# Optimization experiments

Measured on AMD Instinct MI355X. Metric: run time of the kernel, lower is better.

## Reference

```python
import jax, jax.numpy as jnp
import numpy as np

MEM_SLOTS, NUM_HEADS, HEAD_SIZE, KEY_SIZE = 8, 8, 128, 128
MEM_SIZE = NUM_HEADS * HEAD_SIZE  # 1024
NUM_GATES = 2 * MEM_SIZE          # 2048 (gate_style='unit')
B, T, INPUT_SIZE = 128, 32, 1024


def _ln(x, g, b, eps=1e-5):
    m = x.mean(-1, keepdims=True)
    v = ((x - m) ** 2).mean(-1, keepdims=True)
    return (x - m) / jnp.sqrt(v + eps) * g + b


def setup_inputs() -> dict:
    key = jax.random.key(0)
    ks = jax.random.split(key, 12)
    s = 0.02  # weight init scale
    memory = jnp.tile(jnp.eye(MEM_SLOTS, MEM_SIZE, dtype=jnp.float32)[None], (B, 1, 1))
    return {
        'x': jax.random.normal(ks[0], (B, T, INPUT_SIZE), jnp.float32),
        'memory': memory,
        'Wi': s * jax.random.normal(ks[1], (INPUT_SIZE, MEM_SIZE), jnp.float32),
        'bi': jnp.zeros((MEM_SIZE,), jnp.float32),
        'Wq': s * jax.random.normal(ks[2], (MEM_SIZE, KEY_SIZE * NUM_HEADS), jnp.float32),
        'bq': jnp.zeros((KEY_SIZE * NUM_HEADS,), jnp.float32),
        'Wk': s * jax.random.normal(ks[3], (MEM_SIZE, KEY_SIZE * NUM_HEADS), jnp.float32),
        'bk': jnp.zeros((KEY_SIZE * NUM_HEADS,), jnp.float32),
        'Wv': s * jax.random.normal(ks[4], (MEM_SIZE, HEAD_SIZE * NUM_HEADS), jnp.float32),
        'bv': jnp.zeros((HEAD_SIZE * NUM_HEADS,), jnp.float32),
        'Wm': s * jax.random.normal(ks[5], (MEM_SIZE, MEM_SIZE), jnp.float32),
        'bm': jnp.zeros((MEM_SIZE,), jnp.float32),
        'ln1_g': jnp.ones((MEM_SIZE,), jnp.float32),
        'ln1_b': jnp.zeros((MEM_SIZE,), jnp.float32),
        'ln2_g': jnp.ones((MEM_SIZE,), jnp.float32),
        'ln2_b': jnp.zeros((MEM_SIZE,), jnp.float32),
        'rep_w': jax.random.normal(ks[6], (MEM_SIZE,), jnp.float32),
        'Wg': s * jax.random.normal(ks[7], (MEM_SIZE, NUM_GATES), jnp.float32),
        'bg': jnp.zeros((NUM_GATES,), jnp.float32),
        'Wmg': 0.01 * jax.random.normal(ks[8], (MEM_SLOTS, MEM_SIZE, NUM_GATES), jnp.float32),
        'forget_bias': jnp.asarray(1.0, jnp.float32),
        'input_bias': jnp.asarray(0.0, jnp.float32),
    }


def reference(x, memory, Wi, bi, Wq, bq, Wk, bk, Wv, bv, Wm, bm,
              ln1_g, ln1_b, ln2_g, ln2_b, rep_w, Wg, bg, Wmg,
              forget_bias, input_bias):
    Bx, S, D, H, K = x.shape[0], MEM_SLOTS, MEM_SIZE, NUM_HEADS, KEY_SIZE

    def step(mem, xt):                             # mem: (B,S,D), xt: (B,input)
        inp = xt @ Wi + bi                         # input_projector -> (B,D)
        inp_r = inp[:, None, :]                    # (B,1,D)
        # --- multihead attention: q from memory, k/v from projected input ---
        q = (mem @ Wq + bq).reshape(Bx, S, H, K).transpose(0, 2, 1, 3)   # (B,H,S,K)
        k = (inp_r @ Wk + bk).reshape(Bx, 1, H, K).transpose(0, 2, 1, 3)  # (B,H,1,K)
        v = (inp_r @ Wv + bv).reshape(Bx, 1, H, HEAD_SIZE).transpose(0, 2, 1, 3)
        scores = jax.nn.softmax(jnp.einsum('bhsk,bhtk->bhst', q, k), axis=-1)  # unscaled, per source
        att = jnp.einsum('bhst,bhtd->bhsd', scores, v)
        att = att.transpose(0, 2, 1, 3).reshape(Bx, S, D)
        # --- residual + LN, shared-weight 2-layer relu MLP, residual + LN ---
        m1 = _ln(mem + att, ln1_g, ln1_b)
        h = jax.nn.relu(m1 @ Wm + bm)
        h = jax.nn.relu(h @ Wm + bm)               # ModuleList([l]*2) shares weights
        m2 = _ln(m1 + h, ln2_g, ln2_b)
        # --- gates (computed from OLD memory and projected input) ---
        gi = (jax.nn.relu(rep_w * inp_r).mean(axis=1) @ Wg + bg)[:, None, :]  # RepeatLinear
        gm = jnp.einsum('bsd,sdg->bsg', jnp.tanh(mem), Wmg)                    # GroupLinearLayer
        gates = gm + gi                                                        # (B,S,2D)
        ig, fg = jnp.split(gates, 2, axis=-1)
        ig = jax.nn.sigmoid(ig + input_bias)
        fg = jax.nn.sigmoid(fg + forget_bias)
        new_mem = ig * jnp.tanh(m2) + fg * mem
        return new_mem, new_mem.reshape(Bx, S * D)

    final_mem, outs = jax.lax.scan(step, memory, x.transpose(1, 0, 2))
    return outs, final_mem  # outs: (T,B,S*D)
```

## Files before the change

### kernel.cpp

```cpp
#include <hip/hip_runtime.h>
#include <math.h>

#define DMEM   1024
#define NGATES 2048
#define NB     128
#define NT     32

__device__ inline float sigm(float x) { return 1.f / (1.f + __expf(-x)); }

template<int FOLD>
__device__ __forceinline__ void gemm128_core(
    const float* __restrict__ A, int lda, long psA,
    const float* __restrict__ abias,
    const float* __restrict__ rep,
    const float* __restrict__ W, int ldw,
    const float* __restrict__ bias,
    float* __restrict__ C, int ldc,
    int row0, int col0, int kbeg, int kend,
    float (*As)[132], float (*Bs)[132])
{
    const int tid  = threadIdx.x;
    const int tr   = (tid >> 4) << 2, tc = (tid & 15) << 2;
    const int arow = tid >> 1, ah = (tid & 1) * 8;
    const int brow = tid >> 4, bcol = (tid & 15) * 8;

    float4 a0, a1, b0, b1;
    auto LOAD = [&](int k0) {
        const float* ap = A + (long)(row0 + arow) * lda + k0 + ah;
        a0 = *(const float4*)ap;
        a1 = *(const float4*)(ap + 4);
        if (FOLD) {
            float4 p0 = *(const float4*)(ap + psA);
            float4 p1 = *(const float4*)(ap + psA + 4);
            float4 c0 = *(const float4*)(abias + k0 + ah);
            float4 c1 = *(const float4*)(abias + k0 + ah + 4);
            a0.x += p0.x + c0.x; a0.y += p0.y + c0.y;
            a0.z += p0.z + c0.z; a0.w += p0.w + c0.w;
            a1.x += p1.x + c1.x; a1.y += p1.y + c1.y;
            a1.z += p1.z + c1.z; a1.w += p1.w + c1.w;
        }
        if (rep) {
            float4 r0 = *(const float4*)(rep + k0 + ah);
            float4 r1 = *(const float4*)(rep + k0 + ah + 4);
            a0.x = fmaxf(a0.x * r0.x, 0.f); a0.y = fmaxf(a0.y * r0.y, 0.f);
            a0.z = fmaxf(a0.z * r0.z, 0.f); a0.w = fmaxf(a0.w * r0.w, 0.f);
            a1.x = fmaxf(a1.x * r1.x, 0.f); a1.y = fmaxf(a1.y * r1.y, 0.f);
            a1.z = fmaxf(a1.z * r1.z, 0.f); a1.w = fmaxf(a1.w * r1.w, 0.f);
        }
        const float* bp = W + (long)(k0 + brow) * ldw + col0 + bcol;
        b0 = *(const float4*)bp;
        b1 = *(const float4*)(bp + 4);
    };

    float acc[8][8] = {};
    LOAD(kbeg);
    const int NIT = (kend - kbeg) >> 4;
    for (int it = 0; it < NIT; ++it) {
        __syncthreads();
        As[ah + 0][arow] = a0.x; As[ah + 1][arow] = a0.y;
        As[ah + 2][arow] = a0.z; As[ah + 3][arow] = a0.w;
        As[ah + 4][arow] = a1.x; As[ah + 5][arow] = a1.y;
        As[ah + 6][arow] = a1.z; As[ah + 7][arow] = a1.w;
        *(float4*)&Bs[brow][bcol]     = b0;
        *(float4*)&Bs[brow][bcol + 4] = b1;
        __syncthreads();
        if (it + 1 < NIT) LOAD(kbeg + ((it + 1) << 4));
#pragma unroll
        for (int kk = 0; kk < 16; ++kk) {
            float a[8], b[8];
            *(float4*)&a[0] = *(const float4*)&As[kk][tr];
            *(float4*)&a[4] = *(const float4*)&As[kk][64 + tr];
            *(float4*)&b[0] = *(const float4*)&Bs[kk][tc];
            *(float4*)&b[4] = *(const float4*)&Bs[kk][64 + tc];
#pragma unroll
            for (int i = 0; i < 8; ++i)
#pragma unroll
                for (int j = 0; j < 8; ++j)
                    acc[i][j] = fmaf(a[i], b[j], acc[i][j]);
        }
    }

#pragma unroll
    for (int jh = 0; jh < 2; ++jh) {
        int cbase = col0 + jh * 64 + tc;
        float4 bv = make_float4(0.f, 0.f, 0.f, 0.f);
        if (bias) bv = *(const float4*)&bias[cbase];
#pragma unroll
        for (int ih = 0; ih < 2; ++ih) {
#pragma unroll
            for (int i = 0; i < 4; ++i) {
                int row = row0 + ih * 64 + tr + i;
                *(float4*)(C + (long)row * ldc + cbase) =
                    make_float4(acc[ih * 4 + i][jh * 4 + 0] + bv.x,
                                acc[ih * 4 + i][jh * 4 + 1] + bv.y,
                                acc[ih * 4 + i][jh * 4 + 2] + bv.z,
                                acc[ih * 4 + i][jh * 4 + 3] + bv.w);
            }
        }
    }
}

__global__ __launch_bounds__(256)
void gemm_inp(const float* __restrict__ x, const float* __restrict__ Wi,
              float* __restrict__ inpP)
{
    __shared__ float As[16][132];
    __shared__ float Bs[16][132];
    const int bid = blockIdx.x;
    const int kc = bid >> 8, j = bid & 255;
    gemm128_core<0>(x, 1024, 0, nullptr, nullptr, Wi, 1024, nullptr,
                    inpP + (long)kc * 4194304, 1024,
                    (j >> 3) * 128, (j & 7) * 128, kc * 512, kc * 512 + 512,
                    As, Bs);
}

__global__ __launch_bounds__(256)
void vgi_kern(const float* __restrict__ inpP, const float* __restrict__ bi,
              const float* __restrict__ repw,
              const float* __restrict__ Wv, const float* __restrict__ bv,
              float* __restrict__ v,
              const float* __restrict__ Wg, const float* __restrict__ bg,
              float* __restrict__ gi)
{
    __shared__ float As[16][132];
    __shared__ float Bs[16][132];
    const int bid = blockIdx.x;
    const bool isv = bid < 256;
    const int  j   = isv ? bid : bid - 256;
    const int  row0 = isv ? (j >> 3) * 128 : (j >> 4) * 128;
    const int  col0 = isv ? (j & 7) * 128  : (j & 15) * 128;
    gemm128_core<1>(inpP, 1024, 4194304, bi,
                    isv ? nullptr : repw,
                    isv ? Wv : Wg, isv ? 1024 : 2048,
                    isv ? bv : bg,
                    isv ? v : gi, isv ? 1024 : 2048,
                    row0, col0, 0, 1024, As, Bs);
}

template<int AMODE>
__device__ __forceinline__ void gemm64_core(
    const float* __restrict__ A, int lda, long psA,
    const float* __restrict__ abias,
    const float* __restrict__ W, int ldw,
    float* __restrict__ C, int ldc,
    int row0, int col0, int kbeg, int kend,
    float (*As)[68], float (*Bs)[68])
{
    const int tid  = threadIdx.x;
    const int tr   = (tid >> 4) << 2, tc = (tid & 15) << 2;
    const int arow = tid >> 2, aseg = (tid & 3) * 8;
    const int brow = tid >> 3, bcol = (tid & 7) * 8;

    float4 a0, a1, b0, b1;
    auto LOAD = [&](int k0) {
        const float* ap = A + (long)(row0 + arow) * lda + k0 + aseg;
        if (AMODE == 0) {
            a0 = *(const float4*)ap;
            a1 = *(const float4*)(ap + 4);
        } else {
            float4 p0 = *(const float4*)ap;
            float4 p1 = *(const float4*)(ap + psA);
            float4 q0 = *(const float4*)(ap + 4);
            float4 q1 = *(const float4*)(ap + psA + 4);
            float4 c0 = *(const float4*)(abias + k0 + aseg);
            float4 c1 = *(const float4*)(abias + k0 + aseg + 4);
            a0.x = fmaxf(p0.x + p1.x + c0.x, 0.f);
            a0.y = fmaxf(p0.y + p1.y + c0.y, 0.f);
            a0.z = fmaxf(p0.z + p1.z + c0.z, 0.f);
            a0.w = fmaxf(p0.w + p1.w + c0.w, 0.f);
            a1.x = fmaxf(q0.x + q1.x + c1.x, 0.f);
            a1.y = fmaxf(q0.y + q1.y + c1.y, 0.f);
            a1.z = fmaxf(q0.z + q1.z + c1.z, 0.f);
            a1.w = fmaxf(q0.w + q1.w + c1.w, 0.f);
        }
        const float* bp = W + (long)(k0 + brow) * ldw + col0 + bcol;
        b0 = *(const float4*)bp;
        b1 = *(const float4*)(bp + 4);
    };

    float acc[4][4] = {};
    LOAD(kbeg);
    const int NIT = (kend - kbeg) >> 5;
    for (int it = 0; it < NIT; ++it) {
        __syncthreads();
        As[aseg + 0][arow] = a0.x; As[aseg + 1][arow] = a0.y;
        As[aseg + 2][arow] = a0.z; As[aseg + 3][arow] = a0.w;
        As[aseg + 4][arow] = a1.x; As[aseg + 5][arow] = a1.y;
        As[aseg + 6][arow] = a1.z; As[aseg + 7][arow] = a1.w;
        *(float4*)&Bs[brow][bcol]     = b0;
        *(float4*)&Bs[brow][bcol + 4] = b1;
        __syncthreads();
        if (it + 1 < NIT) LOAD(kbeg + ((it + 1) << 5));
#pragma unroll
        for (int kk = 0; kk < 32; ++kk) {
            float4 av = *(const float4*)&As[kk][tr];
            float4 bv = *(const float4*)&Bs[kk][tc];
            acc[0][0] = fmaf(av.x, bv.x, acc[0][0]); acc[0][1] = fmaf(av.x, bv.y, acc[0][1]);
            acc[0][2] = fmaf(av.x, bv.z, acc[0][2]); acc[0][3] = fmaf(av.x, bv.w, acc[0][3]);
            acc[1][0] = fmaf(av.y, bv.x, acc[1][0]); acc[1][1] = fmaf(av.y, bv.y, acc[1][1]);
            acc[1][2] = fmaf(av.y, bv.z, acc[1][2]); acc[1][3] = fmaf(av.y, bv.w, acc[1][3]);
            acc[2][0] = fmaf(av.z, bv.x, acc[2][0]); acc[2][1] = fmaf(av.z, bv.y, acc[2][1]);
            acc[2][2] = fmaf(av.z, bv.z, acc[2][2]); acc[2][3] = fmaf(av.z, bv.w, acc[2][3]);
            acc[3][0] = fmaf(av.w, bv.x, acc[3][0]); acc[3][1] = fmaf(av.w, bv.y, acc[3][1]);
            acc[3][2] = fmaf(av.w, bv.z, acc[3][2]); acc[3][3] = fmaf(av.w, bv.w, acc[3][3]);
        }
    }

#pragma unroll
    for (int i = 0; i < 4; ++i)
        *(float4*)(C + (long)(row0 + tr + i) * ldc + col0 + tc) =
            make_float4(acc[i][0], acc[i][1], acc[i][2], acc[i][3]);
}

template<int LVL>
__global__ __launch_bounds__(256)
void step_gemms(const float* __restrict__ m1, const float* __restrict__ Wm,
                const float* __restrict__ bm,
                float* __restrict__ hP, float* __restrict__ h2P,
                const float* __restrict__ tm, const float* __restrict__ Wmg,
                float* __restrict__ gm)
{
    __shared__ float As[32][68];
    __shared__ float Bs[32][68];
    const int bid = blockIdx.x;
    if (bid < 512) {
        int x = bid & 15, y = (bid >> 4) & 15, kc = bid >> 8;
        if (LVL == 0)
            gemm64_core<0>(m1, 1024, 0, nullptr, Wm, 1024,
                           hP + (long)kc * 1048576, 1024,
                           y * 64, x * 64, kc * 512, kc * 512 + 512, As, Bs);
        else
            gemm64_core<1>(hP, 1024, 1048576, bm, Wm, 1024,
                           h2P + (long)kc * 1048576, 1024,
                           y * 64, x * 64, kc * 512, kc * 512 + 512, As, Bs);
    } else {
        int j = bid - 512;
        int x = (j & 15) + (LVL == 0 ? 0 : 16);
        int y = (j >> 4) & 1, s = j >> 5;
        gemm64_core<0>(tm + s * 1024, 8192, 0, nullptr,
                       Wmg + (long)s * 2097152, 2048,
                       gm + s * 2048, 16384,
                       y * 64, x * 64, 0, 1024, As, Bs);
    }
}

__device__ inline void block_reduce2(float& s1, float& s2)
{
    __shared__ float red[2][4];
    __syncthreads();
#pragma unroll
    for (int off = 32; off > 0; off >>= 1) {
        s1 += __shfl_down(s1, off, 64);
        s2 += __shfl_down(s2, off, 64);
    }
    int tid = threadIdx.x;
    if ((tid & 63) == 0) { red[0][tid >> 6] = s1; red[1][tid >> 6] = s2; }
    __syncthreads();
    s1 = red[0][0] + red[0][1] + red[0][2] + red[0][3];
    s2 = red[1][0] + red[1][1] + red[1][2] + red[1][3];
}

__global__ __launch_bounds__(256)
void ln1_kern(const float* __restrict__ memprev, const float* __restrict__ v,
              const float* __restrict__ g, const float* __restrict__ bb,
              float* __restrict__ m1, float* __restrict__ tm)
{
    const int row = blockIdx.x;
    const int b   = row >> 3;
    const int d   = threadIdx.x << 2;

    float4 mv = *(const float4*)(memprev + (long)row * DMEM + d);
    float4 vv = *(const float4*)(v + ((long)b * NT) * DMEM + d);

    *(float4*)(tm + (long)row * DMEM + d) =
        make_float4(tanhf(mv.x), tanhf(mv.y), tanhf(mv.z), tanhf(mv.w));

    float x0 = mv.x + vv.x, x1 = mv.y + vv.y, x2 = mv.z + vv.z, x3 = mv.w + vv.w;
    float s1 = x0 + x1 + x2 + x3;
    float s2 = x0 * x0 + x1 * x1 + x2 * x2 + x3 * x3;
    block_reduce2(s1, s2);
    float mean = s1 * (1.f / 1024.f);
    float var  = s2 * (1.f / 1024.f) - mean * mean;
    float inv  = 1.f / sqrtf(var + 1e-5f);

    float4 gg = *(const float4*)&g[d];
    float4 bv = *(const float4*)&bb[d];
    *(float4*)(m1 + (long)row * DMEM + d) =
        make_float4((x0 - mean) * inv * gg.x + bv.x,
                    (x1 - mean) * inv * gg.y + bv.y,
                    (x2 - mean) * inv * gg.z + bv.z,
                    (x3 - mean) * inv * gg.w + bv.w);
}

__global__ __launch_bounds__(256)
void step_fused(const float* m1in, const float* __restrict__ h2P,
                const float* __restrict__ bm,
                const float* __restrict__ g2, const float* __restrict__ b2,
                const float* __restrict__ gm, const float* __restrict__ gi, int t,
                const float* __restrict__ memprev,
                const float* __restrict__ fbp, const float* __restrict__ ibp,
                const float* __restrict__ v,
                const float* __restrict__ g1, const float* __restrict__ b1,
                float* __restrict__ outp, float* m1out,
                float* __restrict__ tm, int last)
{
    const int row = blockIdx.x;
    const int b   = row >> 3;
    const int d   = threadIdx.x << 2;
    const long o  = (long)row * DMEM + d;

    float4 a  = *(const float4*)(m1in + o);
    float4 q0 = *(const float4*)(h2P + o);
    float4 q1 = *(const float4*)(h2P + 1048576 + o);
    float4 bb = *(const float4*)&bm[d];
    float x0 = a.x + fmaxf(q0.x + q1.x + bb.x, 0.f);
    float x1 = a.y + fmaxf(q0.y + q1.y + bb.y, 0.f);
    float x2 = a.z + fmaxf(q0.z + q1.z + bb.z, 0.f);
    float x3 = a.w + fmaxf(q0.w + q1.w + bb.w, 0.f);

    float s1 = x0 + x1 + x2 + x3;
    float s2 = x0 * x0 + x1 * x1 + x2 * x2 + x3 * x3;
    block_reduce2(s1, s2);
    float mean = s1 * (1.f / 1024.f);
    float var  = s2 * (1.f / 1024.f) - mean * mean;
    float inv  = 1.f / sqrtf(var + 1e-5f);

    float4 gg = *(const float4*)&g2[d];
    float4 b2v = *(const float4*)&b2[d];
    float t20 = tanhf((x0 - mean) * inv * gg.x + b2v.x);
    float t21 = tanhf((x1 - mean) * inv * gg.y + b2v.y);
    float t22 = tanhf((x2 - mean) * inv * gg.z + b2v.z);
    float t23 = tanhf((x3 - mean) * inv * gg.w + b2v.w);

    const float ib = *ibp, fb = *fbp;
    const long go = (long)row * NGATES + d;
    float4 ge0 = *(const float4*)(gm + go);
    float4 ge1 = *(const float4*)(gm + go + DMEM);
    const long io = ((long)b * NT + t) * NGATES + d;
    float4 i0 = *(const float4*)(gi + io);
    float4 i1 = *(const float4*)(gi + io + DMEM);
    float4 mv = *(const float4*)(memprev + o);

    float4 out;
    out.x = sigm(ge0.x + i0.x + ib) * t20 + sigm(ge1.x + i1.x + fb) * mv.x;
    out.y = sigm(ge0.y + i0.y + ib) * t21 + sigm(ge1.y + i1.y + fb) * mv.y;
    out.z = sigm(ge0.z + i0.z + ib) * t22 + sigm(ge1.z + i1.z + fb) * mv.z;
    out.w = sigm(ge0.w + i0.w + ib) * t23 + sigm(ge1.w + i1.w + fb) * mv.w;
    *(float4*)(outp + o) = out;

    if (!last) {
        float4 vv = *(const float4*)(v + ((long)b * NT + t + 1) * DMEM + d);
        *(float4*)(tm + o) =
            make_float4(tanhf(out.x), tanhf(out.y), tanhf(out.z), tanhf(out.w));

        float y0 = out.x + vv.x, y1 = out.y + vv.y;
        float y2 = out.z + vv.z, y3 = out.w + vv.w;
        float u1 = y0 + y1 + y2 + y3;
        float u2 = y0 * y0 + y1 * y1 + y2 * y2 + y3 * y3;
        block_reduce2(u1, u2);
        float mean1 = u1 * (1.f / 1024.f);
        float var1  = u2 * (1.f / 1024.f) - mean1 * mean1;
        float inv1  = 1.f / sqrtf(var1 + 1e-5f);

        float4 g1v = *(const float4*)&g1[d];
        float4 b1v = *(const float4*)&b1[d];
        *(float4*)(m1out + o) =
            make_float4((y0 - mean1) * inv1 * g1v.x + b1v.x,
                        (y1 - mean1) * inv1 * g1v.y + b1v.y,
                        (y2 - mean1) * inv1 * g1v.z + b1v.z,
                        (y3 - mean1) * inv1 * g1v.w + b1v.w);
    }
}

extern "C" void kernel_launch(void* const* d_in, const int* in_sizes, int n_in,
                              void* d_out, int out_size, void* d_ws, size_t ws_size,
                              hipStream_t stream)
{
    const float* x    = (const float*)d_in[0];
    const float* mem0 = (const float*)d_in[1];
    const float* Wi   = (const float*)d_in[2];
    const float* bi   = (const float*)d_in[3];
    const float* Wv   = (const float*)d_in[8];
    const float* bv   = (const float*)d_in[9];
    const float* Wm   = (const float*)d_in[10];
    const float* bm   = (const float*)d_in[11];
    const float* ln1g = (const float*)d_in[12];
    const float* ln1b = (const float*)d_in[13];
    const float* ln2g = (const float*)d_in[14];
    const float* ln2b = (const float*)d_in[15];
    const float* repw = (const float*)d_in[16];
    const float* Wg   = (const float*)d_in[17];
    const float* bg   = (const float*)d_in[18];
    const float* Wmg  = (const float*)d_in[19];
    const float* fbp  = (const float*)d_in[20];
    const float* ibp  = (const float*)d_in[21];

    float* out = (float*)d_out;
    char*  ws  = (char*)d_ws;
    const long MB = 1024L * 1024L;

    float* v    = (float*)(ws + 0 * MB);
    float* gi   = (float*)(ws + 16 * MB);
    float* inpP = (float*)(ws + 48 * MB);
    float* m1   = (float*)(ws + 48 * MB);
    float* tm   = (float*)(ws + 52 * MB);
    float* hP   = (float*)(ws + 56 * MB);
    float* gm   = (float*)(ws + 64 * MB);
    float* h2P  = (float*)(ws + 72 * MB);

    dim3 blk(256);

    gemm_inp<<<512, blk, 0, stream>>>(x, Wi, inpP);
    vgi_kern<<<768, blk, 0, stream>>>(inpP, bi, repw, Wv, bv, v, Wg, bg, gi);

    ln1_kern<<<1024, blk, 0, stream>>>(mem0, v, ln1g, ln1b, m1, tm);

    const long stepN = (long)NB * 8 * DMEM;
    for (int t = 0; t < NT; ++t) {
        const float* memprev = (t == 0) ? mem0 : out + (long)(t - 1) * stepN;

        step_gemms<0><<<768, blk, 0, stream>>>(m1, Wm, bm, hP, h2P, tm, Wmg, gm);
        step_gemms<1><<<768, blk, 0, stream>>>(m1, Wm, bm, hP, h2P, tm, Wmg, gm);
        step_fused<<<1024, blk, 0, stream>>>(
            m1, h2P, bm, ln2g, ln2b, gm, gi, t, memprev, fbp, ibp,
            v, ln1g, ln1b, out + (long)t * stepN, m1, tm,
            (t == NT - 1) ? 1 : 0);
    }

    hipMemcpyAsync(out + 32L * stepN, out + 31L * stepN, stepN * sizeof(float),
                   hipMemcpyDeviceToDevice, stream);
}
```

Before: 5.283 ms.

## Replace per-step kernel launches with a persistent cooperative kernel using grid syncs

Runs the whole 32-step recurrence inside one cooperative kernel of 768 blocks. Grid-wide barriers separate the two GEMM phases and the LayerNorm/gate tail, replacing 96 separate kernel launches. The final-memory copy is folded into the last step's tail writes instead of a separate memcpy. The cost is grid.sync overhead, tail rows spread unevenly over blocks (1024 rows on 768 blocks), and a fallback to the old launches if the cooperative launch fails.

```diff
diff --git a/kernel.cpp b/kernel.cpp
--- a/kernel.cpp
+++ b/kernel.cpp
@@ -1,10 +1,14 @@
 #include <hip/hip_runtime.h>
+#include <hip/hip_cooperative_groups.h>
 #include <math.h>
+
+namespace cg = cooperative_groups;
 
 #define DMEM   1024
 #define NGATES 2048
 #define NB     128
 #define NT     32
+#define STEPN  1048576L
 
 __device__ inline float sigm(float x) { return 1.f / (1.f + __expf(-x)); }
 
@@ -212,6 +216,205 @@
             make_float4(acc[i][0], acc[i][1], acc[i][2], acc[i][3]);
 }
 
+__device__ inline void block_reduce2(float& s1, float& s2)
+{
+    __shared__ float red[2][4];
+    __syncthreads();
+#pragma unroll
+    for (int off = 32; off > 0; off >>= 1) {
+        s1 += __shfl_down(s1, off, 64);
+        s2 += __shfl_down(s2, off, 64);
+    }
+    int tid = threadIdx.x;
+    if ((tid & 63) == 0) { red[0][tid >> 6] = s1; red[1][tid >> 6] = s2; }
+    __syncthreads();
+    s1 = red[0][0] + red[0][1] + red[0][2] + red[0][3];
+    s2 = red[1][0] + red[1][1] + red[1][2] + red[1][3];
+}
+
+__global__ __launch_bounds__(256)
+void ln1_kern(const float* __restrict__ memprev, const float* __restrict__ v,
+              const float* __restrict__ g, const float* __restrict__ bb,
+              float* __restrict__ m1, float* __restrict__ tm)
+{
+    const int row = blockIdx.x;
+    const int b   = row >> 3;
+    const int d   = threadIdx.x << 2;
+
+    float4 mv = *(const float4*)(memprev + (long)row * DMEM + d);
+    float4 vv = *(const float4*)(v + ((long)b * NT) * DMEM + d);
+
+    *(float4*)(tm + (long)row * DMEM + d) =
+        make_float4(tanhf(mv.x), tanhf(mv.y), tanhf(mv.z), tanhf(mv.w));
+
+    float x0 = mv.x + vv.x, x1 = mv.y + vv.y, x2 = mv.z + vv.z, x3 = mv.w + vv.w;
+    float s1 = x0 + x1 + x2 + x3;
+    float s2 = x0 * x0 + x1 * x1 + x2 * x2 + x3 * x3;
+    block_reduce2(s1, s2);
+    float mean = s1 * (1.f / 1024.f);
+    float var  = s2 * (1.f / 1024.f) - mean * mean;
+    float inv  = 1.f / sqrtf(var + 1e-5f);
+
+    float4 gg = *(const float4*)&g[d];
+    float4 bv = *(const float4*)&bb[d];
+    *(float4*)(m1 + (long)row * DMEM + d) =
+        make_float4((x0 - mean) * inv * gg.x + bv.x,
+                    (x1 - mean) * inv * gg.y + bv.y,
+                    (x2 - mean) * inv * gg.z + bv.z,
+                    (x3 - mean) * inv * gg.w + bv.w);
+}
+
+__device__ __forceinline__ void tail_row(
+    int row, int t, const float* __restrict__ m1in,
+    const float* __restrict__ h2P, const float* __restrict__ bm,
+    const float* __restrict__ g2, const float* __restrict__ b2,
+    const float* __restrict__ gm, const float* __restrict__ gi,
+    const float* __restrict__ memprev, float fb, float ib,
+    const float* __restrict__ v,
+    const float* __restrict__ g1, const float* __restrict__ b1,
+    float* __restrict__ outp, float* m1out, float* __restrict__ tm,
+    int last, float* __restrict__ outFinal)
+{
+    const int b = row >> 3;
+    const int d = threadIdx.x << 2;
+    const long o = (long)row * DMEM + d;
+
+    float4 a  = *(const float4*)(m1in + o);
+    float4 q0 = *(const float4*)(h2P + o);
+    float4 q1 = *(const float4*)(h2P + 1048576 + o);
+    float4 bb = *(const float4*)&bm[d];
+    float x0 = a.x + fmaxf(q0.x + q1.x + bb.x, 0.f);
+    float x1 = a.y + fmaxf(q0.y + q1.y + bb.y, 0.f);
+    float x2 = a.z + fmaxf(q0.z + q1.z + bb.z, 0.f);
+    float x3 = a.w + fmaxf(q0.w + q1.w + bb.w, 0.f);
+
+    float s1 = x0 + x1 + x2 + x3;
+    float s2 = x0 * x0 + x1 * x1 + x2 * x2 + x3 * x3;
+    block_reduce2(s1, s2);
+    float mean = s1 * (1.f / 1024.f);
+    float var  = s2 * (1.f / 1024.f) - mean * mean;
+    float inv  = 1.f / sqrtf(var + 1e-5f);
+
+    float4 gg  = *(const float4*)&g2[d];
+    float4 b2v = *(const float4*)&b2[d];
+    float t20 = tanhf((x0 - mean) * inv * gg.x + b2v.x);
+    float t21 = tanhf((x1 - mean) * inv * gg.y + b2v.y);
+    float t22 = tanhf((x2 - mean) * inv * gg.z + b2v.z);
+    float t23 = tanhf((x3 - mean) * inv * gg.w + b2v.w);
+
+    const long go = (long)row * NGATES + d;
+    float4 ge0 = *(const float4*)(gm + go);
+    float4 ge1 = *(const float4*)(gm + go + DMEM);
+    const long io = ((long)b * NT + t) * NGATES + d;
+    float4 i0 = *(const float4*)(gi + io);
+    float4 i1 = *(const float4*)(gi + io + DMEM);
+    float4 mv = *(const float4*)(memprev + o);
+
+    float4 ov;
+    ov.x = sigm(ge0.x + i0.x + ib) * t20 + sigm(ge1.x + i1.x + fb) * mv.x;
+    ov.y = sigm(ge0.y + i0.y + ib) * t21 + sigm(ge1.y + i1.y + fb) * mv.y;
+    ov.z = sigm(ge0.z + i0.z + ib) * t22 + sigm(ge1.z + i1.z + fb) * mv.z;
+    ov.w = sigm(ge0.w + i0.w + ib) * t23 + sigm(ge1.w + i1.w + fb) * mv.w;
+    *(float4*)(outp + o) = ov;
+
+    if (!last) {
+        float4 vv = *(const float4*)(v + ((long)b * NT + t + 1) * DMEM + d);
+        *(float4*)(tm + o) =
+            make_float4(tanhf(ov.x), tanhf(ov.y), tanhf(ov.z), tanhf(ov.w));
+
+        float y0 = ov.x + vv.x, y1 = ov.y + vv.y;
+        float y2 = ov.z + vv.z, y3 = ov.w + vv.w;
+        float u1 = y0 + y1 + y2 + y3;
+        float u2 = y0 * y0 + y1 * y1 + y2 * y2 + y3 * y3;
+        block_reduce2(u1, u2);
+        float mean1 = u1 * (1.f / 1024.f);
+        float var1  = u2 * (1.f / 1024.f) - mean1 * mean1;
+        float inv1  = 1.f / sqrtf(var1 + 1e-5f);
+
+        float4 g1v = *(const float4*)&g1[d];
+        float4 b1v = *(const float4*)&b1[d];
+        *(float4*)(m1out + o) =
+            make_float4((y0 - mean1) * inv1 * g1v.x + b1v.x,
+                        (y1 - mean1) * inv1 * g1v.y + b1v.y,
+                        (y2 - mean1) * inv1 * g1v.z + b1v.z,
+                        (y3 - mean1) * inv1 * g1v.w + b1v.w);
+    } else {
+        *(float4*)(outFinal + o) = ov;
+    }
+}
+
+__global__ __launch_bounds__(256, 3)
+void scan_kern(const float* __restrict__ mem0,
+               const float* __restrict__ Wm,
+               const float* __restrict__ bm,
+               const float* __restrict__ Wmg,
+               float* __restrict__ hP, float* __restrict__ h2P,
+               float* __restrict__ gm, float* __restrict__ m1,
+               float* __restrict__ tm,
+               const float* __restrict__ v,
+               const float* __restrict__ gi,
+               const float* __restrict__ ln1g,
+               const float* __restrict__ ln1b,
+               const float* __restrict__ ln2g,
+               const float* __restrict__ ln2b,
+               const float* __restrict__ fbp,
+               const float* __restrict__ ibp,
+               float* __restrict__ out)
+{
+    cg::grid_group grid = cg::this_grid();
+    __shared__ float As[32][68];
+    __shared__ float Bs[32][68];
+    const int bid = blockIdx.x;
+    const float fb = *fbp, ib = *ibp;
+
+    for (int t = 0; t < NT; ++t) {
+        const float* memprev = (t == 0) ? mem0 : out + (long)(t - 1) * STEPN;
+
+        {
+            const float* A; int lda; const float* W; int ldw;
+            float* C; int ldc; int r0, c0, kb, ke;
+            if (bid < 512) {
+                int x = bid & 15, y = (bid >> 4) & 15, kc = bid >> 8;
+                A = m1; lda = 1024; W = Wm; ldw = 1024;
+                C = hP + (long)kc * 1048576; ldc = 1024;
+                r0 = y * 64; c0 = x * 64; kb = kc * 512; ke = kb + 512;
+            } else {
+                int j = bid - 512;
+                int x = j & 15, y = (j >> 4) & 1, s = j >> 5;
+                A = tm + s * 1024; lda = 8192;
+                W = Wmg + (long)s * 2097152; ldw = 2048;
+                C = gm + s * 2048; ldc = 16384;
+                r0 = y * 64; c0 = x * 64; kb = 0; ke = 1024;
+            }
+            gemm64_core<0>(A, lda, 0, nullptr, W, ldw, C, ldc,
+                           r0, c0, kb, ke, As, Bs);
+        }
+        grid.sync();
+
+        if (bid < 512) {
+            int x = bid & 15, y = (bid >> 4) & 15, kc = bid >> 8;
+            gemm64_core<1>(hP, 1024, 1048576, bm, Wm, 1024,
+                           h2P + (long)kc * 1048576, 1024,
+                           y * 64, x * 64, kc * 512, kc * 512 + 512, As, Bs);
+        } else {
+            int j = bid - 512;
+            int x = (j & 15) + 16, y = (j >> 4) & 1, s = j >> 5;
+            gemm64_core<0>(tm + s * 1024, 8192, 0, nullptr,
+                           Wmg + (long)s * 2097152, 2048,
+                           gm + s * 2048, 16384,
+                           y * 64, x * 64, 0, 1024, As, Bs);
+        }
+        grid.sync();
+
+        const int last = (t == NT - 1) ? 1 : 0;
+        for (int row = bid; row < 1024; row += 768)
+            tail_row(row, t, m1, h2P, bm, ln2g, ln2b, gm, gi, memprev,
+                     fb, ib, v, ln1g, ln1b, out + (long)t * STEPN, m1, tm,
+                     last, out + (long)NT * STEPN);
+        grid.sync();
+    }
+}
+
 template<int LVL>
 __global__ __launch_bounds__(256)
 void step_gemms(const float* __restrict__ m1, const float* __restrict__ Wm,
@@ -244,54 +447,6 @@
     }
 }
 
-__device__ inline void block_reduce2(float& s1, float& s2)
-{
-    __shared__ float red[2][4];
-    __syncthreads();
-#pragma unroll
-    for (int off = 32; off > 0; off >>= 1) {
-        s1 += __shfl_down(s1, off, 64);
-        s2 += __shfl_down(s2, off, 64);
-    }
-    int tid = threadIdx.x;
-    if ((tid & 63) == 0) { red[0][tid >> 6] = s1; red[1][tid >> 6] = s2; }
-    __syncthreads();
-    s1 = red[0][0] + red[0][1] + red[0][2] + red[0][3];
-    s2 = red[1][0] + red[1][1] + red[1][2] + red[1][3];
-}
-
-__global__ __launch_bounds__(256)
-void ln1_kern(const float* __restrict__ memprev, const float* __restrict__ v,
-              const float* __restrict__ g, const float* __restrict__ bb,
-              float* __restrict__ m1, float* __restrict__ tm)
-{
-    const int row = blockIdx.x;
-    const int b   = row >> 3;
-    const int d   = threadIdx.x << 2;
-
-    float4 mv = *(const float4*)(memprev + (long)row * DMEM + d);
-    float4 vv = *(const float4*)(v + ((long)b * NT) * DMEM + d);
-
-    *(float4*)(tm + (long)row * DMEM + d) =
-        make_float4(tanhf(mv.x), tanhf(mv.y), tanhf(mv.z), tanhf(mv.w));
-
-    float x0 = mv.x + vv.x, x1 = mv.y + vv.y, x2 = mv.z + vv.z, x3 = mv.w + vv.w;
-    float s1 = x0 + x1 + x2 + x3;
-    float s2 = x0 * x0 + x1 * x1 + x2 * x2 + x3 * x3;
-    block_reduce2(s1, s2);
-    float mean = s1 * (1.f / 1024.f);
-    float var  = s2 * (1.f / 1024.f) - mean * mean;
-    float inv  = 1.f / sqrtf(var + 1e-5f);
-
-    float4 gg = *(const float4*)&g[d];
-    float4 bv = *(const float4*)&bb[d];
-    *(float4*)(m1 + (long)row * DMEM + d) =
-        make_float4((x0 - mean) * inv * gg.x + bv.x,
-                    (x1 - mean) * inv * gg.y + bv.y,
-                    (x2 - mean) * inv * gg.z + bv.z,
-                    (x3 - mean) * inv * gg.w + bv.w);
-}
-
 __global__ __launch_bounds__(256)
 void step_fused(const float* m1in, const float* __restrict__ h2P,
                 const float* __restrict__ bm,
@@ -302,74 +457,10 @@
                 const float* __restrict__ v,
                 const float* __restrict__ g1, const float* __restrict__ b1,
                 float* __restrict__ outp, float* m1out,
-                float* __restrict__ tm, int last)
-{
-    const int row = blockIdx.x;
-    const int b   = row >> 3;
-    const int d   = threadIdx.x << 2;
-    const long o  = (long)row * DMEM + d;
-
-    float4 a  = *(const float4*)(m1in + o);
-    float4 q0 = *(const float4*)(h2P + o);
-    float4 q1 = *(const float4*)(h2P + 1048576 + o);
-    float4 bb = *(const float4*)&bm[d];
-    float x0 = a.x + fmaxf(q0.x + q1.x + bb.x, 0.f);
-    float x1 = a.y + fmaxf(q0.y + q1.y + bb.y, 0.f);
-    float x2 = a.z + fmaxf(q0.z + q1.z + bb.z, 0.f);
-    float x3 = a.w + fmaxf(q0.w + q1.w + bb.w, 0.f);
-
-    float s1 = x0 + x1 + x2 + x3;
-    float s2 = x0 * x0 + x1 * x1 + x2 * x2 + x3 * x3;
-    block_reduce2(s1, s2);
-    float mean = s1 * (1.f / 1024.f);
-    float var  = s2 * (1.f / 1024.f) - mean * mean;
-    float inv  = 1.f / sqrtf(var + 1e-5f);
-
-    float4 gg = *(const float4*)&g2[d];
-    float4 b2v = *(const float4*)&b2[d];
-    float t20 = tanhf((x0 - mean) * inv * gg.x + b2v.x);
-    float t21 = tanhf((x1 - mean) * inv * gg.y + b2v.y);
-    float t22 = tanhf((x2 - mean) * inv * gg.z + b2v.z);
-    float t23 = tanhf((x3 - mean) * inv * gg.w + b2v.w);
-
-    const float ib = *ibp, fb = *fbp;
-    const long go = (long)row * NGATES + d;
-    float4 ge0 = *(const float4*)(gm + go);
-    float4 ge1 = *(const float4*)(gm + go + DMEM);
-    const long io = ((long)b * NT + t) * NGATES + d;
-    float4 i0 = *(const float4*)(gi + io);
-    float4 i1 = *(const float4*)(gi + io + DMEM);
-    float4 mv = *(const float4*)(memprev + o);
-
-    float4 out;
-    out.x = sigm(ge0.x + i0.x + ib) * t20 + sigm(ge1.x + i1.x + fb) * mv.x;
-    out.y = sigm(ge0.y + i0.y + ib) * t21 + sigm(ge1.y + i1.y + fb) * mv.y;
-    out.z = sigm(ge0.z + i0.z + ib) * t22 + sigm(ge1.z + i1.z + fb) * mv.z;
-    out.w = sigm(ge0.w + i0.w + ib) * t23 + sigm(ge1.w + i1.w + fb) * mv.w;
-    *(float4*)(outp + o) = out;
-
-    if (!last) {
-        float4 vv = *(const float4*)(v + ((long)b * NT + t + 1) * DMEM + d);
-        *(float4*)(tm + o) =
-            make_float4(tanhf(out.x), tanhf(out.y), tanhf(out.z), tanhf(out.w));
-
-        float y0 = out.x + vv.x, y1 = out.y + vv.y;
-        float y2 = out.z + vv.z, y3 = out.w + vv.w;
-        float u1 = y0 + y1 + y2 + y3;
-        float u2 = y0 * y0 + y1 * y1 + y2 * y2 + y3 * y3;
-        block_reduce2(u1, u2);
-        float mean1 = u1 * (1.f / 1024.f);
-        float var1  = u2 * (1.f / 1024.f) - mean1 * mean1;
-        float inv1  = 1.f / sqrtf(var1 + 1e-5f);
-
-        float4 g1v = *(const float4*)&g1[d];
-        float4 b1v = *(const float4*)&b1[d];
-        *(float4*)(m1out + o) =
-            make_float4((y0 - mean1) * inv1 * g1v.x + b1v.x,
-                        (y1 - mean1) * inv1 * g1v.y + b1v.y,
-                        (y2 - mean1) * inv1 * g1v.z + b1v.z,
-                        (y3 - mean1) * inv1 * g1v.w + b1v.w);
-    }
+                float* __restrict__ tm, int last, float* __restrict__ outFinal)
+{
+    tail_row(blockIdx.x, t, m1in, h2P, bm, g2, b2, gm, gi, memprev,
+             *fbp, *ibp, v, g1, b1, outp, m1out, tm, last, outFinal);
 }
 
 extern "C" void kernel_launch(void* const* d_in, const int* in_sizes, int n_in,
@@ -415,18 +506,25 @@
 
     ln1_kern<<<1024, blk, 0, stream>>>(mem0, v, ln1g, ln1b, m1, tm);
 
-    const long stepN = (long)NB * 8 * DMEM;
-    for (int t = 0; t < NT; ++t) {
-        const float* memprev = (t == 0) ? mem0 : out + (long)(t - 1) * stepN;
-
-        step_gemms<0><<<768, blk, 0, stream>>>(m1, Wm, bm, hP, h2P, tm, Wmg, gm);
-        step_gemms<1><<<768, blk, 0, stream>>>(m1, Wm, bm, hP, h2P, tm, Wmg, gm);
-        step_fused<<<1024, blk, 0, stream>>>(
-            m1, h2P, bm, ln2g, ln2b, gm, gi, t, memprev, fbp, ibp,
-            v, ln1g, ln1b, out + (long)t * stepN, m1, tm,
-            (t == NT - 1) ? 1 : 0);
-    }
-
-    hipMemcpyAsync(out + 32L * stepN, out + 31L * stepN, stepN * sizeof(float),
-                   hipMemcpyDeviceToDevice, stream);
-}
+    void* args[] = {
+        (void*)&mem0, (void*)&Wm, (void*)&bm, (void*)&Wmg,
+        (void*)&hP, (void*)&h2P, (void*)&gm, (void*)&m1, (void*)&tm,
+        (void*)&v, (void*)&gi,
+        (void*)&ln1g, (void*)&ln1b, (void*)&ln2g, (void*)&ln2b,
+        (void*)&fbp, (void*)&ibp, (void*)&out
+    };
+    hipError_t cerr = hipLaunchCooperativeKernel((void*)scan_kern, dim3(768),
+                                                 dim3(256), args, 0, stream);
+    if (cerr != hipSuccess) {
+        (void)hipGetLastError();
+        for (int t = 0; t < NT; ++t) {
+            const float* memprev = (t == 0) ? mem0 : out + (long)(t - 1) * STEPN;
+            step_gemms<0><<<768, blk, 0, stream>>>(m1, Wm, bm, hP, h2P, tm, Wmg, gm);
+            step_gemms<1><<<768, blk, 0, stream>>>(m1, Wm, bm, hP, h2P, tm, Wmg, gm);
+            step_fused<<<1024, blk, 0, stream>>>(
+                m1, h2P, bm, ln2g, ln2b, gm, gi, t, memprev, fbp, ibp,
+                v, ln1g, ln1b, out + (long)t * STEPN, m1, tm,
+                (t == NT - 1) ? 1 : 0, out + (long)NT * STEPN);
+        }
+    }
+}
```

New measurement: 13.96 ms. +164.2%, slower.
